# Optimization experiments

Hardware: AMD Instinct MI355X
Metric: run time of the kernel (lower is better)

Reference implementation:

```python
import jax, jax.numpy as jnp
import numpy as np

EMBED_DIM = 1024
NUM_HEADS = 16
HEAD_DIM = EMBED_DIM // NUM_HEADS
MLP_HIDDEN = 4096
B, S = 2, 2048


def setup_inputs() -> dict:
    key = jax.random.key(0)
    ks = jax.random.split(key, 10)
    sd = lambda fan_in: 1.0 / np.sqrt(fan_in)
    x = jax.random.normal(ks[0], (B, S, EMBED_DIM), dtype=jnp.float32)
    # weights stored (in, out) so y = x @ W + b (same math as torch Linear)
    w_qkv = jax.random.normal(ks[1], (EMBED_DIM, 3 * EMBED_DIM), jnp.float32) * sd(EMBED_DIM)
    w_proj = jax.random.normal(ks[2], (EMBED_DIM, EMBED_DIM), jnp.float32) * sd(EMBED_DIM)
    b_proj = jnp.zeros((EMBED_DIM,), jnp.float32)
    w_fc1 = jax.random.normal(ks[3], (EMBED_DIM, MLP_HIDDEN), jnp.float32) * sd(EMBED_DIM)
    b_fc1 = jnp.zeros((MLP_HIDDEN,), jnp.float32)
    w_fc2 = jax.random.normal(ks[4], (MLP_HIDDEN, EMBED_DIM), jnp.float32) * sd(MLP_HIDDEN)
    b_fc2 = jnp.zeros((EMBED_DIM,), jnp.float32)
    g1 = jnp.ones((EMBED_DIM,), jnp.float32)
    be1 = jnp.zeros((EMBED_DIM,), jnp.float32)
    g2 = jnp.ones((EMBED_DIM,), jnp.float32)
    be2 = jnp.zeros((EMBED_DIM,), jnp.float32)
    return {"x": x, "w_qkv": w_qkv, "w_proj": w_proj, "b_proj": b_proj,
            "w_fc1": w_fc1, "b_fc1": b_fc1, "w_fc2": w_fc2, "b_fc2": b_fc2,
            "g1": g1, "be1": be1, "g2": g2, "be2": be2}


def _layernorm(x, g, b, eps=1e-5):
    mu = jnp.mean(x, axis=-1, keepdims=True)
    var = jnp.var(x, axis=-1, keepdims=True)
    return (x - mu) * jax.lax.rsqrt(var + eps) * g + b


def _block(x, w_qkv, w_proj, b_proj, w_fc1, b_fc1, w_fc2, b_fc2, g1, be1, g2, be2):
    # --- attention branch ---
    h = _layernorm(x, g1, be1)
    qkv = h @ w_qkv  # [B,S,3D]
    qkv = qkv.reshape(B, S, 3, NUM_HEADS, HEAD_DIM).transpose(2, 0, 3, 1, 4)
    q, k, v = qkv[0], qkv[1], qkv[2]  # each [B,H,S,Dh]
    scale = 1.0 / np.sqrt(HEAD_DIM).astype(np.float32)
    dots = jnp.einsum('bhqd,bhkd->bhqk', q, k) * scale  # naive full score matrix
    attn = jax.nn.softmax(dots, axis=-1)
    out = jnp.einsum('bhqk,bhkd->bhqd', attn, v)
    out = out.transpose(0, 2, 1, 3).reshape(B, S, EMBED_DIM)
    x = x + (out @ w_proj + b_proj)
    # --- mlp branch ---
    h2 = _layernorm(x, g2, be2)
    mlp = jax.nn.gelu(h2 @ w_fc1 + b_fc1, approximate=False) @ w_fc2 + b_fc2
    return x + mlp


def reference(x, w_qkv, w_proj, b_proj, w_fc1, b_fc1, w_fc2, b_fc2, g1, be1, g2, be2):
    return _block(x, w_qkv, w_proj, b_proj, w_fc1, b_fc1, w_fc2, b_fc2, g1, be1, g2, be2)
```

## Files before the change

kernel.cpp:

```cpp
#include <hip/hip_runtime.h>

typedef __attribute__((ext_vector_type(8))) short short8;
typedef __attribute__((ext_vector_type(4))) float f32x4;

#define MFMA16(a, b, c) __builtin_amdgcn_mfma_f32_16x16x32_bf16((a), (b), (c), 0, 0, 0)

static __device__ __forceinline__ unsigned short f2bf(float f) {
    unsigned int u = __float_as_uint(f);
    return (unsigned short)((u + 0x7fffu + ((u >> 16) & 1u)) >> 16);
}

static __device__ __forceinline__ void glds16(const unsigned short* g, unsigned short* l) {
    __builtin_amdgcn_global_load_lds(
        (const __attribute__((address_space(1))) unsigned int*)g,
        (__attribute__((address_space(3))) unsigned int*)l, 16, 0, 0);
}

__global__ __launch_bounds__(256) void convt_all_kernel(
    const float* __restrict__ w_qkv, const float* __restrict__ w_proj,
    const float* __restrict__ w_fc1, const float* __restrict__ w_fc2,
    unsigned short* __restrict__ wqkvT, unsigned short* __restrict__ wprojT,
    unsigned short* __restrict__ wfc1T, unsigned short* __restrict__ wfc2T) {
    __shared__ unsigned short Ts[32][33];
    int id = blockIdx.x;
    const float* W; unsigned short* WT; int K, N, bx, by;
    if (id < 3072)      { W = w_qkv;  WT = wqkvT;  K = 1024; N = 3072; bx = id % 96;  by = id / 96; }
    else if (id < 4096) { id -= 3072; W = w_proj; WT = wprojT; K = 1024; N = 1024; bx = id & 31; by = id >> 5; }
    else if (id < 8192) { id -= 4096; W = w_fc1;  WT = wfc1T;  K = 1024; N = 4096; bx = id & 127; by = id >> 7; }
    else                { id -= 8192; W = w_fc2;  WT = wfc2T;  K = 4096; N = 1024; bx = id & 31; by = id >> 5; }
    int t = threadIdx.x;
    int bk = by * 32, bn = bx * 32;
    int r = t >> 3, c = (t & 7) * 4;
    float4 w = *(const float4*)&W[(size_t)(bk + r) * N + bn + c];
    Ts[c + 0][r] = f2bf(w.x); Ts[c + 1][r] = f2bf(w.y);
    Ts[c + 2][r] = f2bf(w.z); Ts[c + 3][r] = f2bf(w.w);
    __syncthreads();
    ushort4 o;
    o.x = Ts[r][c]; o.y = Ts[r][c + 1]; o.z = Ts[r][c + 2]; o.w = Ts[r][c + 3];
    *(ushort4*)&WT[(size_t)(bn + r) * K + bk + c] = o;
}

__global__ __launch_bounds__(256) void ln_kernel(const float* __restrict__ x,
                                                 const float* __restrict__ g,
                                                 const float* __restrict__ be,
                                                 unsigned short* __restrict__ y) {
    int row = blockIdx.x;
    const float* xr = x + (size_t)row * 1024;
    unsigned short* yr = y + (size_t)row * 1024;
    int t = threadIdx.x;
    float v[4];
    float sum = 0.f, sq = 0.f;
#pragma unroll
    for (int i = 0; i < 4; ++i) {
        float f = xr[t + i * 256];
        v[i] = f; sum += f; sq += f * f;
    }
#pragma unroll
    for (int o = 32; o > 0; o >>= 1) { sum += __shfl_down(sum, o); sq += __shfl_down(sq, o); }
    __shared__ float red[8];
    int wave = t >> 6, lane = t & 63;
    if (lane == 0) { red[wave] = sum; red[4 + wave] = sq; }
    __syncthreads();
    sum = red[0] + red[1] + red[2] + red[3];
    sq  = red[4] + red[5] + red[6] + red[7];
    float mean = sum * (1.f / 1024.f);
    float var  = sq * (1.f / 1024.f) - mean * mean;
    float rstd = rsqrtf(var + 1e-5f);
#pragma unroll
    for (int i = 0; i < 4; ++i) {
        int c = t + i * 256;
        yr[c] = f2bf((v[i] - mean) * rstd * g[c] + be[c]);
    }
}

template <int BN>
__global__ __launch_bounds__(256) void gemm_kernel(const unsigned short* __restrict__ A,
                                                   const unsigned short* __restrict__ BT,
                                                   const float* __restrict__ bias,
                                                   const float* __restrict__ resid,
                                                   void* __restrict__ C,
                                                   int M, int N, int K, int act, int cF32) {
    constexpr int NT = BN / 32;
    __shared__ __align__(16) unsigned short As[2][128][32];
    __shared__ __align__(16) unsigned short Bs[2][BN][32];
    int t = threadIdx.x, wave = t >> 6, lane = t & 63;
    int lm = lane & 15, quad = lane >> 4;
    int wm = (wave >> 1) * 64, wn = (wave & 1) * (BN / 2);

    int id = blockIdx.y * gridDim.x + blockIdx.x;
    int gsz = gridDim.x * 8;
    int grp = id / gsz, rem = id % gsz;
    int br = (grp * 8 + (rem & 7)) * 128;
    int bc = (rem >> 3) * BN;

    int srow = lane >> 2;
    int scol = ((lane & 3) ^ ((srow >> 1) & 3)) * 8;
    const unsigned short* Ag0 = A + (size_t)(br + wave * 32 + srow) * K + scol;
    const unsigned short* Ag1 = Ag0 + (size_t)16 * K;
    const unsigned short* Bg0 = BT + (size_t)(bc + wave * (BN / 4) + srow) * K + scol;
    const unsigned short* Bg1 = Bg0 + (size_t)16 * K;

    f32x4 zero4 = {0.f, 0.f, 0.f, 0.f};
    f32x4 acc[4][NT];
#pragma unroll
    for (int i = 0; i < 4; ++i)
#pragma unroll
        for (int j = 0; j < NT; ++j) acc[i][j] = zero4;

    auto stage = [&](int buf, int ko) {
        glds16(Ag0 + ko, &As[buf][wave * 32][0]);
        glds16(Ag1 + ko, &As[buf][wave * 32 + 16][0]);
        glds16(Bg0 + ko, &Bs[buf][wave * (BN / 4)][0]);
        if (BN == 128) glds16(Bg1 + ko, &Bs[buf][wave * (BN / 4) + 16][0]);
    };

    int nt = K >> 5;
    stage(0, 0);
    int rsw = (lm >> 1) & 3;
    int cq = (quad ^ rsw) << 3;
    for (int tt = 0; tt < nt; ++tt) {
        int cur = tt & 1;
        if (tt + 1 < nt) {
            stage(cur ^ 1, (tt + 1) << 5);
            if (BN == 128) asm volatile("s_waitcnt vmcnt(4)" ::: "memory");
            else           asm volatile("s_waitcnt vmcnt(3)" ::: "memory");
        } else {
            asm volatile("s_waitcnt vmcnt(0)" ::: "memory");
        }
        __builtin_amdgcn_s_barrier();
        __builtin_amdgcn_sched_barrier(0);
        short8 af[4], bf[NT];
#pragma unroll
        for (int i = 0; i < 4; ++i) af[i] = *(const short8*)&As[cur][wm + i * 16 + lm][cq];
#pragma unroll
        for (int j = 0; j < NT; ++j) bf[j] = *(const short8*)&Bs[cur][wn + j * 16 + lm][cq];
#pragma unroll
        for (int i = 0; i < 4; ++i)
#pragma unroll
            for (int j = 0; j < NT; ++j) acc[i][j] = MFMA16(af[i], bf[j], acc[i][j]);
        __builtin_amdgcn_sched_barrier(0);
        __builtin_amdgcn_s_barrier();
    }

#pragma unroll
    for (int i = 0; i < 4; ++i)
#pragma unroll
        for (int j = 0; j < NT; ++j) {
            int col = bc + wn + j * 16 + lm;
            float bv = bias ? bias[col] : 0.f;
#pragma unroll
            for (int r = 0; r < 4; ++r) {
                int row = br + wm + i * 16 + quad * 4 + r;
                float v = acc[i][j][r] + bv;
                if (act == 1) v = 0.5f * v * (1.f + erff(v * 0.70710678118f));
                size_t idx = (size_t)row * N + col;
                if (resid) v += resid[idx];
                if (cF32) ((float*)C)[idx] = v;
                else ((unsigned short*)C)[idx] = f2bf(v);
            }
        }
}

__global__ __launch_bounds__(256) void kvprep_kernel(const unsigned short* __restrict__ qkv,
                                                     unsigned short* __restrict__ Kp,
                                                     unsigned short* __restrict__ Vt) {
    __shared__ unsigned short Vl[64][72];
    int t = threadIdx.x;
    int w = blockIdx.x, bh = blockIdx.y;
    int b = bh >> 4, h = bh & 15;
    int kt = w * 64;
    int sl = t >> 2, c = (t & 3) * 16;
    const unsigned short* src = qkv + (size_t)(b * 2048 + kt + sl) * 3072 + h * 64 + c;
    {
        uint4 k0 = *(const uint4*)(src + 1024);
        uint4 k1 = *(const uint4*)(src + 1024 + 8);
        int sw = sl & 7;
        int o0 = (c >> 3), o1 = o0 + 1;
        unsigned short* krow = Kp + ((size_t)bh * 2048 + kt + sl) * 64;
        *(uint4*)&krow[(o0 ^ sw) << 3] = k0;
        *(uint4*)&krow[(o1 ^ sw) << 3] = k1;
    }
    {
        uint4 v0 = *(const uint4*)(src + 2048);
        uint4 v1 = *(const uint4*)(src + 2048 + 8);
        *(uint4*)&Vl[sl][c] = v0;
        *(uint4*)&Vl[sl][c + 8] = v1;
    }
    __syncthreads();
    {
        int d = t >> 2, kc = (t & 3) * 16;
        unsigned short vv[16];
#pragma unroll
        for (int i = 0; i < 16; ++i) vv[i] = Vl[kc + i][d];
        int sw = d & 7;
        int ko0 = kc >> 3, ko1 = ko0 + 1;
        unsigned short* vrow = Vt + ((((size_t)bh * 32 + w) * 64) + d) * 64;
        *(uint4*)&vrow[(ko0 ^ sw) << 3] = *(uint4*)&vv[0];
        *(uint4*)&vrow[(ko1 ^ sw) << 3] = *(uint4*)&vv[8];
    }
}

__global__ __launch_bounds__(256) void attn2_kernel(const unsigned short* __restrict__ qkv,
                                                    const unsigned short* __restrict__ Kp,
                                                    const unsigned short* __restrict__ Vt,
                                                    unsigned short* __restrict__ out) {
    __shared__ __align__(16) unsigned short Qs[64][72];
    __shared__ __align__(16) unsigned short Ks[4096];
    __shared__ __align__(16) unsigned short Vs[4096];
    __shared__ __align__(16) unsigned short Ps[4][16][72];

    int t = threadIdx.x, wave = t >> 6, lane = t & 63;
    int lm = lane & 15, quad = lane >> 4, k8 = quad * 8;
    int bh = blockIdx.y, b = bh >> 4, h = bh & 15;
    int q0 = blockIdx.x * 64;
    const unsigned short* base = qkv + (size_t)b * 2048 * 3072 + h * 64;

    {
        int r = t >> 2, c = (t & 3) * 16;
        const unsigned short* src = base + (size_t)(q0 + r) * 3072 + c;
        *(uint4*)&Qs[r][c] = *(const uint4*)src;
        *(uint4*)&Qs[r][c + 8] = *(const uint4*)(src + 8);
    }
    __syncthreads();
    short8 qa0 = *(const short8*)&Qs[wave * 16 + lm][k8];
    short8 qa1 = *(const short8*)&Qs[wave * 16 + lm][32 + k8];

    f32x4 zero4 = {0.f, 0.f, 0.f, 0.f};
    f32x4 oacc[4] = {zero4, zero4, zero4, zero4};
    float lsum[4] = {0.f, 0.f, 0.f, 0.f};

    for (int kt = 0; kt < 2048; kt += 64) {
        __syncthreads();
        {
            const unsigned short* kg = Kp + ((size_t)bh * 2048 + kt) * 64 + wave * 1024 + (lane << 3);
            unsigned short* kl = &Ks[wave * 1024];
            glds16(kg, kl);
            glds16(kg + 512, kl + 512);
            const unsigned short* vg = Vt + (((size_t)bh * 32 + (kt >> 6)) * 64) * 64 + wave * 1024 + (lane << 3);
            unsigned short* vl = &Vs[wave * 1024];
            glds16(vg, vl);
            glds16(vg + 512, vl + 512);
        }
        __syncthreads();

        f32x4 s[4];
#pragma unroll
        for (int nt = 0; nt < 4; ++nt) {
            int key = nt * 16 + lm;
            int swk = lm & 7;
            const unsigned short* krow = &Ks[key * 64];
            short8 kf0 = *(const short8*)&krow[(quad ^ swk) << 3];
            short8 kf1 = *(const short8*)&krow[((quad ^ swk) ^ 4) << 3];
            f32x4 a = zero4;
            a = MFMA16(qa0, kf0, a);
            a = MFMA16(qa1, kf1, a);
            s[nt] = a;
        }

#pragma unroll
        for (int r = 0; r < 4; ++r) {
            int row = quad * 4 + r;
            int sw = (row >> 1) & 7;
#pragma unroll
            for (int nt = 0; nt < 4; ++nt) {
                float p = __expf(s[nt][r] * 0.125f - 8.0f);
                lsum[r] += p;
                int g = (nt << 1) + (lm >> 3);
                Ps[wave][row][((g ^ sw) << 3) + (lm & 7)] = f2bf(p);
            }
        }

#pragma unroll
        for (int kh = 0; kh < 2; ++kh) {
            int pg = (kh << 2) + quad;
            short8 pa = *(const short8*)&Ps[wave][lm][(pg ^ ((lm >> 1) & 7)) << 3];
#pragma unroll
            for (int nt = 0; nt < 4; ++nt) {
                int d = nt * 16 + lm;
                short8 vf = *(const short8*)&Vs[d * 64 + ((pg ^ (lm & 7)) << 3)];
                oacc[nt] = MFMA16(pa, vf, oacc[nt]);
            }
        }
    }

#pragma unroll
    for (int r = 0; r < 4; ++r) {
        float l = lsum[r];
        l += __shfl_xor(l, 1); l += __shfl_xor(l, 2);
        l += __shfl_xor(l, 4); l += __shfl_xor(l, 8);
        float inv = 1.f / l;
        int qrow = q0 + wave * 16 + quad * 4 + r;
        size_t o = ((size_t)(b * 2048 + qrow)) * 1024 + h * 64;
#pragma unroll
        for (int nt = 0; nt < 4; ++nt) out[o + nt * 16 + lm] = f2bf(oacc[nt][r] * inv);
    }
}

__global__ __launch_bounds__(256) void attn_kernel(const unsigned short* __restrict__ qkv,
                                                   unsigned short* __restrict__ out) {
    __shared__ __align__(16) unsigned short Qs[64][72];
    __shared__ __align__(16) unsigned short Ks[64][72];
    __shared__ __align__(16) unsigned short Vs[64][72];
    __shared__ __align__(16) unsigned short Ps[4][16][72];
    int t = threadIdx.x, wave = t >> 6, lane = t & 63;
    int lm = lane & 15, quad = lane >> 4, k8 = quad * 8;
    int bh = blockIdx.y, b = bh >> 4, h = bh & 15;
    int q0 = blockIdx.x * 64;
    const unsigned short* base = qkv + (size_t)b * 2048 * 3072 + h * 64;
    const unsigned short* kb = base + 1024;
    const unsigned short* vb = base + 2048;
    {
        int r = t >> 2, c = (t & 3) * 16;
        const unsigned short* src = base + (size_t)(q0 + r) * 3072 + c;
        *(uint4*)&Qs[r][c] = *(const uint4*)src;
        *(uint4*)&Qs[r][c + 8] = *(const uint4*)(src + 8);
    }
    __syncthreads();
    short8 qa0 = *(const short8*)&Qs[wave * 16 + lm][k8];
    short8 qa1 = *(const short8*)&Qs[wave * 16 + lm][32 + k8];
    f32x4 zero4 = {0.f, 0.f, 0.f, 0.f};
    f32x4 oacc[4] = {zero4, zero4, zero4, zero4};
    float lsum[4] = {0.f, 0.f, 0.f, 0.f};
    int sr = t >> 2, sc = (t & 3) * 16;
    for (int kt = 0; kt < 2048; kt += 64) {
        __syncthreads();
        {
            const unsigned short* ksrc = kb + (size_t)(kt + sr) * 3072 + sc;
            *(uint4*)&Ks[sr][sc] = *(const uint4*)ksrc;
            *(uint4*)&Ks[sr][sc + 8] = *(const uint4*)(ksrc + 8);
            const unsigned short* vsrc = vb + (size_t)(kt + sr) * 3072 + sc;
            unsigned short tv[16] __attribute__((aligned(16)));
            *(uint4*)&tv[0] = *(const uint4*)vsrc;
            *(uint4*)&tv[8] = *(const uint4*)(vsrc + 8);
            int kg = sr >> 3, kw = sr & 7;
#pragma unroll
            for (int j = 0; j < 16; ++j) {
                int d = sc + j;
                Vs[d][((kg ^ ((d >> 3) & 7)) << 3) + kw] = tv[j];
            }
        }
        __syncthreads();
        f32x4 s[4];
#pragma unroll
        for (int nt = 0; nt < 4; ++nt) {
            short8 kf0 = *(const short8*)&Ks[nt * 16 + lm][k8];
            short8 kf1 = *(const short8*)&Ks[nt * 16 + lm][32 + k8];
            f32x4 a = zero4;
            a = MFMA16(qa0, kf0, a);
            a = MFMA16(qa1, kf1, a);
            s[nt] = a;
        }
#pragma unroll
        for (int r = 0; r < 4; ++r) {
            int row = quad * 4 + r;
            int sw = (row >> 1) & 7;
#pragma unroll
            for (int nt = 0; nt < 4; ++nt) {
                float p = __expf(s[nt][r] * 0.125f - 8.0f);
                lsum[r] += p;
                int g = (nt << 1) + (lm >> 3);
                Ps[wave][row][((g ^ sw) << 3) + (lm & 7)] = f2bf(p);
            }
        }
#pragma unroll
        for (int kh = 0; kh < 2; ++kh) {
            int pg = (kh << 2) + quad;
            short8 pa = *(const short8*)&Ps[wave][lm][(pg ^ ((lm >> 1) & 7)) << 3];
#pragma unroll
            for (int nt = 0; nt < 4; ++nt) {
                int d = nt * 16 + lm;
                short8 vf = *(const short8*)&Vs[d][(pg ^ ((d >> 3) & 7)) << 3];
                oacc[nt] = MFMA16(pa, vf, oacc[nt]);
            }
        }
    }
#pragma unroll
    for (int r = 0; r < 4; ++r) {
        float l = lsum[r];
        l += __shfl_xor(l, 1); l += __shfl_xor(l, 2);
        l += __shfl_xor(l, 4); l += __shfl_xor(l, 8);
        float inv = 1.f / l;
        int qrow = q0 + wave * 16 + quad * 4 + r;
        size_t o = ((size_t)(b * 2048 + qrow)) * 1024 + h * 64;
#pragma unroll
        for (int nt = 0; nt < 4; ++nt) out[o + nt * 16 + lm] = f2bf(oacc[nt][r] * inv);
    }
}

extern "C" void kernel_launch(void* const* d_in, const int* in_sizes, int n_in,
                              void* d_out, int out_size, void* d_ws, size_t ws_size,
                              hipStream_t stream) {
    const float* x      = (const float*)d_in[0];
    const float* w_qkv  = (const float*)d_in[1];
    const float* w_proj = (const float*)d_in[2];
    const float* b_proj = (const float*)d_in[3];
    const float* w_fc1  = (const float*)d_in[4];
    const float* b_fc1  = (const float*)d_in[5];
    const float* w_fc2  = (const float*)d_in[6];
    const float* b_fc2  = (const float*)d_in[7];
    const float* g1     = (const float*)d_in[8];
    const float* be1    = (const float*)d_in[9];
    const float* g2     = (const float*)d_in[10];
    const float* be2    = (const float*)d_in[11];
    float* out = (float*)d_out;
    unsigned short* sb = (unsigned short*)d_out;

    char* ws = (char*)d_ws;
    unsigned short* wqkvT  = (unsigned short*)ws;
    unsigned short* wprojT = (unsigned short*)(ws + ((size_t)6u << 20));
    unsigned short* wfc1T  = (unsigned short*)(ws + ((size_t)8u << 20));
    unsigned short* wfc2T  = (unsigned short*)(ws + ((size_t)16u << 20));
    unsigned short* qkv    = (unsigned short*)(ws + ((size_t)24u << 20));

    convt_all_kernel<<<dim3(12288), dim3(256), 0, stream>>>(
        w_qkv, w_proj, w_fc1, w_fc2, wqkvT, wprojT, wfc1T, wfc2T);
    ln_kernel<<<dim3(4096), dim3(256), 0, stream>>>(x, g1, be1, sb);
    gemm_kernel<128><<<dim3(24, 32), dim3(256), 0, stream>>>(
        sb, wqkvT, nullptr, nullptr, qkv, 4096, 3072, 1024, 0, 0);

    if (ws_size >= ((size_t)72u << 20)) {
        unsigned short* Kp = (unsigned short*)(ws + ((size_t)48u << 20));
        unsigned short* Vt = (unsigned short*)(ws + ((size_t)56u << 20));
        float*          x2 = (float*)(ws + ((size_t)24u << 20));
        unsigned short* m1 = (unsigned short*)(ws + ((size_t)40u << 20));
        kvprep_kernel<<<dim3(32, 32), dim3(256), 0, stream>>>(qkv, Kp, Vt);
        attn2_kernel<<<dim3(32, 32), dim3(256), 0, stream>>>(qkv, Kp, Vt, sb);
        gemm_kernel<64><<<dim3(16, 32), dim3(256), 0, stream>>>(
            sb, wprojT, b_proj, x, x2, 4096, 1024, 1024, 0, 1);
        ln_kernel<<<dim3(4096), dim3(256), 0, stream>>>(x2, g2, be2, sb);
        gemm_kernel<128><<<dim3(32, 32), dim3(256), 0, stream>>>(
            sb, wfc1T, b_fc1, nullptr, m1, 4096, 4096, 1024, 1, 0);
        gemm_kernel<64><<<dim3(16, 32), dim3(256), 0, stream>>>(
            m1, wfc2T, b_fc2, x2, out, 4096, 1024, 4096, 0, 1);
    } else {
        float*          x2  = (float*)(ws + ((size_t)24u << 20));
        unsigned short* m1c = (unsigned short*)(ws + ((size_t)40u << 20));
        unsigned short* h2  = (unsigned short*)d_out + ((size_t)4u << 20);
        attn_kernel<<<dim3(32, 32), dim3(256), 0, stream>>>(qkv, sb);
        gemm_kernel<64><<<dim3(16, 32), dim3(256), 0, stream>>>(
            sb, wprojT, b_proj, x, x2, 4096, 1024, 1024, 0, 1);
        ln_kernel<<<dim3(4096), dim3(256), 0, stream>>>(x2, g2, be2, h2);
        for (int c = 0; c < 4; ++c) {
            size_t ro = (size_t)c * 1024;
            gemm_kernel<128><<<dim3(32, 8), dim3(256), 0, stream>>>(
                h2 + ro * 1024, wfc1T, b_fc1, nullptr, m1c, 1024, 4096, 1024, 1, 0);
            gemm_kernel<64><<<dim3(16, 8), dim3(256), 0, stream>>>(
                m1c, wfc2T, b_fc2, x2 + ro * 1024, out + ro * 1024, 1024, 1024, 4096, 0, 1);
        }
    }
}
```

Before: 416.9 us.

## Add 256x256-tile 4-stage pipelined GEMM for QKV and FC1 projections

Introduces a 512-thread GEMM kernel with 256x256 output tiles and a 4-deep global-to-LDS prefetch ring using explicit vmcnt waits. It is used for the QKV and FC1 matmuls in place of the 128-wide tile kernel. The larger tiles raise arithmetic intensity and cut redundant global loads, and the deeper pipeline hides memory latency. In exchange it uses 128 KB of LDS and many accumulator registers, and the QKV grid (192 blocks) underfills the CU count.

Result: slower. 451.4 us (+8.3%).

```diff
diff --git a/kernel.cpp b/kernel.cpp
--- a/kernel.cpp
+++ b/kernel.cpp
@@ -73,6 +73,96 @@
     }
 }
 
+__global__ __launch_bounds__(512) void gemm256_kernel(const unsigned short* __restrict__ A,
+                                                      const unsigned short* __restrict__ BT,
+                                                      const float* __restrict__ bias,
+                                                      const float* __restrict__ resid,
+                                                      void* __restrict__ C,
+                                                      int M, int N, int K, int act, int cF32) {
+    __shared__ __align__(16) unsigned short As[4][256][32];
+    __shared__ __align__(16) unsigned short Bs[4][256][32];
+    int t = threadIdx.x, wave = t >> 6, lane = t & 63;
+    int lm = lane & 15, quad = lane >> 4;
+    int wm = (wave >> 2) * 128, wn = (wave & 3) * 64;
+
+    int id = blockIdx.y * gridDim.x + blockIdx.x;
+    int gsz = gridDim.x * 8;
+    int grp = id / gsz, rem = id % gsz;
+    int br = (grp * 8 + (rem & 7)) * 256;
+    int bc = (rem >> 3) * 256;
+
+    int srow = lane >> 2;
+    int scol = ((lane & 3) ^ ((srow >> 1) & 3)) * 8;
+    const unsigned short* Ag0 = A + (size_t)(br + wave * 32 + srow) * K + scol;
+    const unsigned short* Ag1 = Ag0 + (size_t)16 * K;
+    const unsigned short* Bg0 = BT + (size_t)(bc + wave * 32 + srow) * K + scol;
+    const unsigned short* Bg1 = Bg0 + (size_t)16 * K;
+
+    f32x4 zero4 = {0.f, 0.f, 0.f, 0.f};
+    f32x4 acc[8][4];
+#pragma unroll
+    for (int i = 0; i < 8; ++i)
+#pragma unroll
+        for (int j = 0; j < 4; ++j) acc[i][j] = zero4;
+
+    auto stage = [&](int buf, int ko) {
+        glds16(Ag0 + ko, &As[buf][wave * 32][0]);
+        glds16(Ag1 + ko, &As[buf][wave * 32 + 16][0]);
+        glds16(Bg0 + ko, &Bs[buf][wave * 32][0]);
+        glds16(Bg1 + ko, &Bs[buf][wave * 32 + 16][0]);
+    };
+
+    int nt = K >> 5;
+    stage(0, 0);
+    stage(1, 32);
+    stage(2, 64);
+    int cq = (quad ^ ((lm >> 1) & 3)) << 3;
+    for (int tt = 0; tt < nt; ++tt) {
+        int cur = tt & 3;
+        if (tt + 3 < nt) {
+            stage((tt + 3) & 3, (tt + 3) << 5);
+            asm volatile("s_waitcnt vmcnt(12)" ::: "memory");
+        } else if (tt + 2 < nt) {
+            asm volatile("s_waitcnt vmcnt(8)" ::: "memory");
+        } else if (tt + 1 < nt) {
+            asm volatile("s_waitcnt vmcnt(4)" ::: "memory");
+        } else {
+            asm volatile("s_waitcnt vmcnt(0)" ::: "memory");
+        }
+        __builtin_amdgcn_s_barrier();
+        __builtin_amdgcn_sched_barrier(0);
+        short8 af[8], bf[4];
+#pragma unroll
+        for (int i = 0; i < 8; ++i) af[i] = *(const short8*)&As[cur][wm + i * 16 + lm][cq];
+#pragma unroll
+        for (int j = 0; j < 4; ++j) bf[j] = *(const short8*)&Bs[cur][wn + j * 16 + lm][cq];
+#pragma unroll
+        for (int i = 0; i < 8; ++i)
+#pragma unroll
+            for (int j = 0; j < 4; ++j) acc[i][j] = MFMA16(af[i], bf[j], acc[i][j]);
+        __builtin_amdgcn_sched_barrier(0);
+        __builtin_amdgcn_s_barrier();
+    }
+
+#pragma unroll
+    for (int i = 0; i < 8; ++i)
+#pragma unroll
+        for (int j = 0; j < 4; ++j) {
+            int col = bc + wn + j * 16 + lm;
+            float bv = bias ? bias[col] : 0.f;
+#pragma unroll
+            for (int r = 0; r < 4; ++r) {
+                int row = br + wm + i * 16 + quad * 4 + r;
+                float v = acc[i][j][r] + bv;
+                if (act == 1) v = 0.5f * v * (1.f + erff(v * 0.70710678118f));
+                size_t idx = (size_t)row * N + col;
+                if (resid) v += resid[idx];
+                if (cF32) ((float*)C)[idx] = v;
+                else ((unsigned short*)C)[idx] = f2bf(v);
+            }
+        }
+}
+
 template <int BN>
 __global__ __launch_bounds__(256) void gemm_kernel(const unsigned short* __restrict__ A,
                                                    const unsigned short* __restrict__ BT,
@@ -415,7 +505,7 @@
     convt_all_kernel<<<dim3(12288), dim3(256), 0, stream>>>(
         w_qkv, w_proj, w_fc1, w_fc2, wqkvT, wprojT, wfc1T, wfc2T);
     ln_kernel<<<dim3(4096), dim3(256), 0, stream>>>(x, g1, be1, sb);
-    gemm_kernel<128><<<dim3(24, 32), dim3(256), 0, stream>>>(
+    gemm256_kernel<<<dim3(12, 16), dim3(512), 0, stream>>>(
         sb, wqkvT, nullptr, nullptr, qkv, 4096, 3072, 1024, 0, 0);
 
     if (ws_size >= ((size_t)72u << 20)) {
@@ -428,7 +518,7 @@
         gemm_kernel<64><<<dim3(16, 32), dim3(256), 0, stream>>>(
             sb, wprojT, b_proj, x, x2, 4096, 1024, 1024, 0, 1);
         ln_kernel<<<dim3(4096), dim3(256), 0, stream>>>(x2, g2, be2, sb);
-        gemm_kernel<128><<<dim3(32, 32), dim3(256), 0, stream>>>(
+        gemm256_kernel<<<dim3(16, 16), dim3(512), 0, stream>>>(
             sb, wfc1T, b_fc1, nullptr, m1, 4096, 4096, 1024, 1, 0);
         gemm_kernel<64><<<dim3(16, 32), dim3(256), 0, stream>>>(
             m1, wfc2T, b_fc2, x2, out, 4096, 1024, 4096, 0, 1);
```
